# Kernel optimization log

Measured on AMD Instinct MI355X. Metric: run time of the kernel, lower is better.

The kernel has to match this reference:

```python
import jax, jax.numpy as jnp
import numpy as np

B, N, P, D, H = 16, 256, 8, 512, 8
E = P * D  # 4096, flattened patch embedding width


def _sincos_pos_embed(q_len, d_model):
    # PatchTST-style 'sincos' positional encoding (learn_pe=False buffer)
    pe = np.zeros((q_len, d_model), dtype=np.float64)
    position = np.arange(q_len, dtype=np.float64)[:, None]
    div_term = np.exp(np.arange(0, d_model, 2, dtype=np.float64) * -(np.log(10000.0) / d_model))
    pe[:, 0::2] = np.sin(position * div_term)
    pe[:, 1::2] = np.cos(position * div_term)
    pe = pe - pe.mean()
    pe = pe / (pe.std() * 10)
    return jnp.asarray(pe, dtype=jnp.float32)


def setup_inputs() -> dict:
    key = jax.random.key(0)
    ks = jax.random.split(key, 10)
    s = 0.02
    return {
        "x": jax.random.normal(ks[0], (B, N, P, D), dtype=jnp.float32),
        "pos_embed": _sincos_pos_embed(N, E),
        "W_embed": jax.random.normal(ks[1], (E, E), dtype=jnp.float32) * s,
        "b_embed": jnp.zeros((E,), dtype=jnp.float32),
        "Wq": jax.random.normal(ks[2], (E, E), dtype=jnp.float32) * s,
        "bq": jnp.zeros((E,), dtype=jnp.float32),
        "Wk": jax.random.normal(ks[3], (E, E), dtype=jnp.float32) * s,
        "bk": jnp.zeros((E,), dtype=jnp.float32),
        "Wv": jax.random.normal(ks[4], (E, E), dtype=jnp.float32) * s,
        "bv": jnp.zeros((E,), dtype=jnp.float32),
        "Wo": jax.random.normal(ks[5], (E, E), dtype=jnp.float32) * s,
        "bo": jnp.zeros((E,), dtype=jnp.float32),
    }


def reference(x, pos_embed, W_embed, b_embed, Wq, bq, Wk, bk, Wv, bv, Wo, bo):
    b, n, p, d = x.shape
    h = H
    dh = E // h  # per-head dim = patch_size * d_keys
    xe = x.reshape(b, n, p * d)                       # B N (P D)
    xe = xe @ W_embed.T + b_embed                     # embed_linear
    xe = xe + pos_embed                               # pos embed (dropout=0, eval)
    q = (xe @ Wq.T + bq).reshape(b, n, h, dh)
    k = (xe @ Wk.T + bk).reshape(b, n, h, dh)
    v = (xe @ Wv.T + bv).reshape(b, n, h, dh)
    scale = 1.0 / np.sqrt(d // h)                     # NOTE: uses d_model//H, not E//H (faithful)
    attn_scores = jnp.einsum('bnhd,bmhd->bhnm', q, k) * scale
    attn_weights = jax.nn.softmax(attn_scores, axis=-1)
    out = jnp.einsum('bhnm,bmhd->bnhd', attn_weights, v).reshape(b, n, h * dh)
    out = out @ Wo.T + bo
    out = out.reshape(b, n, p, d)
    return out, attn_weights
```

## Files before the change

### kernel.cpp

```cpp
#include <hip/hip_runtime.h>
#include <hip/hip_bf16.h>


typedef unsigned short u16;
typedef _Float16 f16;
typedef __attribute__((ext_vector_type(8))) _Float16 v8h;
typedef __attribute__((ext_vector_type(8))) short vu16x8;
typedef __attribute__((ext_vector_type(4))) float vf32x4;

#define MFMA_F16(a, b, c) __builtin_amdgcn_mfma_f32_16x16x32_f16(a, b, c, 0, 0, 0)

__device__ __forceinline__ void gld16(const void* g, void* l) {
    __builtin_amdgcn_global_load_lds((const __attribute__((address_space(1))) void*)g,
                                     (__attribute__((address_space(3))) void*)l,
                                     16, 0, 0);
}

__global__ __launch_bounds__(256) void tof16(const float* __restrict__ s,
                                             f16* __restrict__ d) {
    const size_t i = ((size_t)blockIdx.x * 256 + threadIdx.x) * 4;
    const float4 v = *(const float4*)(s + i);
    d[i + 0] = (f16)v.x; d[i + 1] = (f16)v.y;
    d[i + 2] = (f16)v.z; d[i + 3] = (f16)v.w;
}

template <int MODE>
__global__ __launch_bounds__(512, 2)
void gemm8_nt(const f16* __restrict__ A, const f16* __restrict__ Bw,
              const float* __restrict__ bias, const float* __restrict__ pos,
              f16* __restrict__ Ch, float* __restrict__ Cf) {
    __shared__ __align__(16) u16 sA[2][16384];
    __shared__ __align__(16) u16 sB[2][16384];
    const int t = threadIdx.x;
    const int lane = t & 63, w = t >> 6;
    const int wm = w >> 2, wn = w & 3;
    const int l15 = lane & 15, lg = lane >> 4;
    const int wg = ((blockIdx.x & 7) << 5) + (blockIdx.x >> 3);
    const int m0 = (wg >> 4) << 8, n0 = (wg & 15) << 8;

    int srow[4], scol[4];
#pragma unroll
    for (int i = 0; i < 4; ++i) {
        const int c = t + (i << 9);
        srow[i] = c >> 3;
        scol[i] = (((c & 7) ^ (srow[i] & 7)) << 3);
    }
    const int rA = (wm << 7) + l15;
    const int rB = (wn << 6) + l15;
    const int xA = rA & 7, xB = rB & 7;

    vf32x4 acc[8][4] = {};

#define STAGE(buf, k0) do {                                                    \
    _Pragma("unroll")                                                          \
    for (int i = 0; i < 4; ++i) {                                              \
        const int c = t + (i << 9);                                            \
        gld16(A  + (((size_t)(m0 + srow[i])) << 12) + (k0) + scol[i],          \
              &sA[buf][c * 8]);                                                \
    }                                                                          \
    _Pragma("unroll")                                                          \
    for (int i = 0; i < 4; ++i) {                                              \
        const int c = t + (i << 9);                                            \
        gld16(Bw + (((size_t)(n0 + srow[i])) << 12) + (k0) + scol[i],          \
              &sB[buf][c * 8]);                                                \
    }                                                                          \
} while (0)

    STAGE(0, 0);

    for (int kt = 0; kt < 64; ++kt) {
        const int cb = kt & 1;
        if (kt < 63) {
            STAGE(cb ^ 1, (kt + 1) << 6);
            asm volatile("s_waitcnt vmcnt(8)" ::: "memory");
        } else {
            asm volatile("s_waitcnt vmcnt(0)" ::: "memory");
        }
        __builtin_amdgcn_s_barrier();
        asm volatile("" ::: "memory");
#pragma unroll
        for (int kk = 0; kk < 2; ++kk) {
            const int ccA = (((kk << 2) + lg) ^ xA) << 3;
            const int ccB = (((kk << 2) + lg) ^ xB) << 3;
            v8h av[8], bv[4];
#pragma unroll
            for (int m = 0; m < 8; ++m)
                av[m] = *(const v8h*)(&sA[cb][(rA << 6) + (m << 10) + ccA]);
#pragma unroll
            for (int n = 0; n < 4; ++n)
                bv[n] = *(const v8h*)(&sB[cb][(rB << 6) + (n << 10) + ccB]);
            asm volatile("s_waitcnt lgkmcnt(0)" ::: "memory");
            __builtin_amdgcn_sched_barrier(0);
            __builtin_amdgcn_s_setprio(1);
#pragma unroll
            for (int m = 0; m < 8; ++m)
#pragma unroll
                for (int n = 0; n < 4; ++n)
                    acc[m][n] = MFMA_F16(av[m], bv[n], acc[m][n]);
            __builtin_amdgcn_s_setprio(0);
        }
        __builtin_amdgcn_s_barrier();
        asm volatile("" ::: "memory");
    }
#undef STAGE

#pragma unroll
    for (int n = 0; n < 4; ++n) {
        const int col = n0 + (wn << 6) + (n << 4) + l15;
        const float bvv = bias[col];
#pragma unroll
        for (int m = 0; m < 8; ++m) {
#pragma unroll
            for (int r = 0; r < 4; ++r) {
                const int row = m0 + (wm << 7) + (m << 4) + (lg << 2) + r;
                float v = acc[m][n][r] + bvv;
                if (MODE == 0) v += pos[((size_t)(row & 255) << 12) + col];
                if (MODE == 2)
                    Cf[((size_t)row << 12) + col] = v;
                else
                    Ch[((size_t)row << 12) + col] = (f16)v;
            }
        }
    }
}

__global__ __launch_bounds__(256)
void attn_scores(const f16* __restrict__ q, const f16* __restrict__ k,
                 float* __restrict__ Pf, f16* __restrict__ Pb) {
    const int blk = ((blockIdx.x & 7) << 6) + (blockIdx.x >> 3);
    const int bh = blk >> 2, it = blk & 3;
    const int b = bh >> 3, h = bh & 7;
    const size_t qoff = ((size_t)(b * 256 + it * 64) << 12) + (h << 9);
    const size_t koff = ((size_t)(b * 256) << 12) + (h << 9);
    __shared__ __align__(16) u16 Qs[64 * 64];
    __shared__ __align__(16) u16 Ks[256 * 64];
    __shared__ float red[4][64];

    const int t = threadIdx.x;
    const int lane = t & 63, w = t >> 6;
    const int l15 = lane & 15, lg = lane >> 4;

    vf32x4 acc[4][4] = {};

    for (int k0 = 0; k0 < 512; k0 += 64) {
#pragma unroll
        for (int i = 0; i < 2; ++i) {
            const int c = t + (i << 8);
            const int row = c >> 3, c8 = (c & 7) << 3;
            gld16(q + qoff + ((size_t)row << 12) + k0 + c8, Qs + c * 8);
        }
#pragma unroll
        for (int i = 0; i < 8; ++i) {
            const int c = t + (i << 8);
            const int row = c >> 3, c8 = (c & 7) << 3;
            gld16(k + koff + ((size_t)row << 12) + k0 + c8, Ks + c * 8);
        }
        __syncthreads();
#pragma unroll
        for (int kk = 0; kk < 2; ++kk) {
            v8h af[4], bf[4];
#pragma unroll
            for (int m = 0; m < 4; ++m)
                af[m] = *(const v8h*)(Qs + (m * 16 + l15) * 64 + kk * 32 + lg * 8);
#pragma unroll
            for (int n = 0; n < 4; ++n)
                bf[n] = *(const v8h*)(Ks + (w * 64 + n * 16 + l15) * 64 + kk * 32 + lg * 8);
#pragma unroll
            for (int m = 0; m < 4; ++m)
#pragma unroll
                for (int n = 0; n < 4; ++n)
                    acc[m][n] = MFMA_F16(af[m], bf[n], acc[m][n]);
        }
        __syncthreads();
    }

#pragma unroll
    for (int m = 0; m < 4; ++m)
#pragma unroll
        for (int n = 0; n < 4; ++n) acc[m][n] *= 0.125f;

    float gm[4][4];
#pragma unroll
    for (int m = 0; m < 4; ++m)
#pragma unroll
        for (int r = 0; r < 4; ++r) {
            float v = fmaxf(fmaxf(acc[m][0][r], acc[m][1][r]),
                            fmaxf(acc[m][2][r], acc[m][3][r]));
#pragma unroll
            for (int off = 1; off < 16; off <<= 1) v = fmaxf(v, __shfl_xor(v, off));
            gm[m][r] = v;
        }
    if (l15 == 0) {
#pragma unroll
        for (int m = 0; m < 4; ++m)
#pragma unroll
            for (int r = 0; r < 4; ++r) red[w][m * 16 + lg * 4 + r] = gm[m][r];
    }
    __syncthreads();
#pragma unroll
    for (int m = 0; m < 4; ++m)
#pragma unroll
        for (int r = 0; r < 4; ++r) {
            const int row = m * 16 + lg * 4 + r;
            gm[m][r] = fmaxf(fmaxf(red[0][row], red[1][row]),
                             fmaxf(red[2][row], red[3][row]));
        }
    __syncthreads();

    float gs[4][4];
#pragma unroll
    for (int m = 0; m < 4; ++m)
#pragma unroll
        for (int r = 0; r < 4; ++r) {
            float s = 0.f;
#pragma unroll
            for (int n = 0; n < 4; ++n) {
                const float e = __expf(acc[m][n][r] - gm[m][r]);
                acc[m][n][r] = e;
                s += e;
            }
#pragma unroll
            for (int off = 1; off < 16; off <<= 1) s += __shfl_xor(s, off);
            gs[m][r] = s;
        }
    if (l15 == 0) {
#pragma unroll
        for (int m = 0; m < 4; ++m)
#pragma unroll
            for (int r = 0; r < 4; ++r) red[w][m * 16 + lg * 4 + r] = gs[m][r];
    }
    __syncthreads();

    const size_t pbase = ((size_t)bh * 256 + it * 64) * 256;
#pragma unroll
    for (int m = 0; m < 4; ++m)
#pragma unroll
        for (int r = 0; r < 4; ++r) {
            const int row = m * 16 + lg * 4 + r;
            const float inv = 1.0f / (red[0][row] + red[1][row] +
                                      red[2][row] + red[3][row]);
#pragma unroll
            for (int n = 0; n < 4; ++n) {
                const int col = w * 64 + n * 16 + l15;
                const float p = acc[m][n][r] * inv;
                Pf[pbase + (size_t)row * 256 + col] = p;
                Pb[pbase + (size_t)row * 256 + col] = (f16)p;
            }
        }
}

__global__ __launch_bounds__(256)
void attn_pv(const f16* __restrict__ P, const f16* __restrict__ V,
             f16* __restrict__ O) {
    __shared__ __align__(16) u16 Ps[128 * 64];
    __shared__ __align__(16) u16 Vt[128 * 72];
    const int t = threadIdx.x;
    const int lane = t & 63, w = t >> 6;
    const int wr = (w >> 1) << 6, wc = (w & 1) << 6;
    const int l15 = lane & 15, lg = lane >> 4;
    const int blk = ((blockIdx.x & 7) << 7) + (blockIdx.x >> 3);
    const int bh = blk >> 3, mt = (blk >> 2) & 1, nt = blk & 3;
    const int b = bh >> 3, h = bh & 7;
    const f16* Pbp = P + ((size_t)bh << 16) + ((size_t)mt << 15);
    const u16* Vb = (const u16*)V + ((size_t)(b * 256) << 12) + (h << 9) + (nt << 7);

    vf32x4 acc[4][4] = {};

    for (int k0 = 0; k0 < 256; k0 += 64) {
#pragma unroll
        for (int i = 0; i < 4; ++i) {
            const int c = t + (i << 8);
            const int row = c >> 3, c8 = (c & 7) << 3;
            gld16(Pbp + (size_t)row * 256 + k0 + c8, Ps + c * 8);
        }
#pragma unroll
        for (int pp = 0; pp < 4; ++pp) {
            const int kr = pp * 16 + (t >> 4);
            const int c8 = (t & 15) << 3;
            vu16x8 vv = *(const vu16x8*)(Vb + ((size_t)(k0 + kr) << 12) + c8);
#pragma unroll
            for (int c = 0; c < 8; ++c) Vt[(c8 + c) * 72 + kr] = (u16)vv[c];
        }
        __syncthreads();
#pragma unroll
        for (int kk = 0; kk < 2; ++kk) {
            v8h af[4], bf[4];
#pragma unroll
            for (int m = 0; m < 4; ++m)
                af[m] = *(const v8h*)(Ps + (wr + m * 16 + l15) * 64 + kk * 32 + lg * 8);
#pragma unroll
            for (int n = 0; n < 4; ++n)
                bf[n] = *(const v8h*)(Vt + (wc + n * 16 + l15) * 72 + kk * 32 + lg * 8);
#pragma unroll
            for (int m = 0; m < 4; ++m)
#pragma unroll
                for (int n = 0; n < 4; ++n)
                    acc[m][n] = MFMA_F16(af[m], bf[n], acc[m][n]);
        }
        __syncthreads();
    }

#pragma unroll
    for (int m = 0; m < 4; ++m)
#pragma unroll
        for (int n = 0; n < 4; ++n) {
            const int col = (h << 9) + (nt << 7) + wc + n * 16 + l15;
#pragma unroll
            for (int r = 0; r < 4; ++r) {
                const int row = b * 256 + mt * 128 + wr + m * 16 + lg * 4 + r;
                O[((size_t)row << 12) + col] = (f16)acc[m][n][r];
            }
        }
}

extern "C" void kernel_launch(void* const* d_in, const int* in_sizes, int n_in,
                              void* d_out, int out_size, void* d_ws, size_t ws_size,
                              hipStream_t stream) {
    const float* x   = (const float*)d_in[0];
    const float* pos = (const float*)d_in[1];
    const float* wE  = (const float*)d_in[2];
    const float* bE  = (const float*)d_in[3];
    const float* wQ  = (const float*)d_in[4];
    const float* bq  = (const float*)d_in[5];
    const float* wK  = (const float*)d_in[6];
    const float* bk  = (const float*)d_in[7];
    const float* wV  = (const float*)d_in[8];
    const float* bv  = (const float*)d_in[9];
    const float* wO  = (const float*)d_in[10];
    const float* bo  = (const float*)d_in[11];

    float* out  = (float*)d_out;
    float* Pout = out + (size_t)16777216;

    char* W = (char*)d_ws;
    const size_t MB = 1024 * 1024;
    f16* xf    = (f16*)(W + 0 * MB);
    f16* wslab = (f16*)(W + 32 * MB);
    f16* xe    = (f16*)(W + 64 * MB);
    f16* qs    = (f16*)(W + 96 * MB);
    f16* ks    = (f16*)(W + 128 * MB);
    f16* vs    = (f16*)(W + 160 * MB);
    f16* Pb    = (f16*)(W + 192 * MB);
    f16* ao    = xf;

    const int CVG = 16384;

    tof16<<<CVG, 256, 0, stream>>>(x, xf);
    tof16<<<CVG, 256, 0, stream>>>(wE, wslab);
    gemm8_nt<0><<<256, 512, 0, stream>>>(xf, wslab, bE, pos, xe, nullptr);

    tof16<<<CVG, 256, 0, stream>>>(wQ, wslab);
    gemm8_nt<1><<<256, 512, 0, stream>>>(xe, wslab, bq, nullptr, qs, nullptr);

    tof16<<<CVG, 256, 0, stream>>>(wK, wslab);
    gemm8_nt<1><<<256, 512, 0, stream>>>(xe, wslab, bk, nullptr, ks, nullptr);

    tof16<<<CVG, 256, 0, stream>>>(wV, wslab);
    gemm8_nt<1><<<256, 512, 0, stream>>>(xe, wslab, bv, nullptr, vs, nullptr);

    attn_scores<<<512, 256, 0, stream>>>(qs, ks, Pout, Pb);
    attn_pv<<<1024, 256, 0, stream>>>(Pb, vs, ao);

    tof16<<<CVG, 256, 0, stream>>>(wO, wslab);
    gemm8_nt<2><<<256, 512, 0, stream>>>(ao, wslab, bo, nullptr, nullptr, out);
}
```

Measured before the change: 859.0 us.

## Fuse next weight's fp16 conversion into the tail of each GEMM kernel

Each projection GEMM now converts the next layer's fp32 weight to fp16 after its epilogue, so four separate tof16 launches go away. Separate weight buffers are assigned so the conversion target never aliases the weight the current GEMM is reading. q is staged in the output buffer as scratch. This trims launch overhead and lets conversion traffic overlap with compute-tail imbalance, at the cost of a longer per-block tail and extra memory use.

New measurement: 873.6 us. About the same (+1.7%).

```diff
diff --git a/kernel.cpp b/kernel.cpp
--- a/kernel.cpp
+++ b/kernel.cpp
@@ -24,11 +24,12 @@
     d[i + 2] = (f16)v.z; d[i + 3] = (f16)v.w;
 }
 
-template <int MODE>
+template <int MODE, bool CVT>
 __global__ __launch_bounds__(512, 2)
 void gemm8_nt(const f16* __restrict__ A, const f16* __restrict__ Bw,
               const float* __restrict__ bias, const float* __restrict__ pos,
-              f16* __restrict__ Ch, float* __restrict__ Cf) {
+              f16* __restrict__ Ch, float* __restrict__ Cf,
+              const float* __restrict__ cvsrc, f16* __restrict__ cvdst) {
     __shared__ __align__(16) u16 sA[2][16384];
     __shared__ __align__(16) u16 sB[2][16384];
     const int t = threadIdx.x;
@@ -120,6 +121,17 @@
                 else
                     Ch[((size_t)row << 12) + col] = (f16)v;
             }
+        }
+    }
+
+    if (CVT) {
+        const size_t g = (size_t)blockIdx.x * 512 + t;
+#pragma unroll 4
+        for (int j = 0; j < 32; ++j) {
+            const size_t i = ((size_t)j * 131072 + g) * 4;
+            const float4 v = *(const float4*)(cvsrc + i);
+            cvdst[i + 0] = (f16)v.x; cvdst[i + 1] = (f16)v.y;
+            cvdst[i + 2] = (f16)v.z; cvdst[i + 3] = (f16)v.w;
         }
     }
 }
@@ -334,33 +346,35 @@
 
     char* W = (char*)d_ws;
     const size_t MB = 1024 * 1024;
-    f16* xf    = (f16*)(W + 0 * MB);
-    f16* wslab = (f16*)(W + 32 * MB);
-    f16* xe    = (f16*)(W + 64 * MB);
-    f16* qs    = (f16*)(W + 96 * MB);
-    f16* ks    = (f16*)(W + 128 * MB);
-    f16* vs    = (f16*)(W + 160 * MB);
-    f16* Pb    = (f16*)(W + 192 * MB);
-    f16* ao    = xf;
+    f16* xf  = (f16*)(W + 0 * MB);
+    f16* wEs = (f16*)(W + 32 * MB);
+    f16* wVs = wEs;
+    f16* xe  = (f16*)(W + 64 * MB);
+    f16* wQs = (f16*)(W + 96 * MB);
+    f16* ao  = wQs;
+    f16* wKs = (f16*)(W + 128 * MB);
+    f16* wOs = wKs;
+    f16* ks  = (f16*)(W + 160 * MB);
+    f16* vs  = (f16*)(W + 192 * MB);
+    f16* Pb  = (f16*)(W + 224 * MB);
+    f16* qs  = (f16*)out;
 
     const int CVG = 16384;
 
     tof16<<<CVG, 256, 0, stream>>>(x, xf);
-    tof16<<<CVG, 256, 0, stream>>>(wE, wslab);
-    gemm8_nt<0><<<256, 512, 0, stream>>>(xf, wslab, bE, pos, xe, nullptr);
-
-    tof16<<<CVG, 256, 0, stream>>>(wQ, wslab);
-    gemm8_nt<1><<<256, 512, 0, stream>>>(xe, wslab, bq, nullptr, qs, nullptr);
-
-    tof16<<<CVG, 256, 0, stream>>>(wK, wslab);
-    gemm8_nt<1><<<256, 512, 0, stream>>>(xe, wslab, bk, nullptr, ks, nullptr);
-
-    tof16<<<CVG, 256, 0, stream>>>(wV, wslab);
-    gemm8_nt<1><<<256, 512, 0, stream>>>(xe, wslab, bv, nullptr, vs, nullptr);
+    tof16<<<CVG, 256, 0, stream>>>(wE, wEs);
+    gemm8_nt<0, true><<<256, 512, 0, stream>>>(xf, wEs, bE, pos, xe, nullptr,
+                                               wQ, wQs);
+    gemm8_nt<1, true><<<256, 512, 0, stream>>>(xe, wQs, bq, nullptr, qs, nullptr,
+                                               wK, wKs);
+    gemm8_nt<1, true><<<256, 512, 0, stream>>>(xe, wKs, bk, nullptr, ks, nullptr,
+                                               wV, wVs);
+    gemm8_nt<1, true><<<256, 512, 0, stream>>>(xe, wVs, bv, nullptr, vs, nullptr,
+                                               wO, wOs);
 
     attn_scores<<<512, 256, 0, stream>>>(qs, ks, Pout, Pb);
     attn_pv<<<1024, 256, 0, stream>>>(Pb, vs, ao);
 
-    tof16<<<CVG, 256, 0, stream>>>(wO, wslab);
-    gemm8_nt<2><<<256, 512, 0, stream>>>(ao, wslab, bo, nullptr, nullptr, out);
-}
+    gemm8_nt<2, false><<<256, 512, 0, stream>>>(ao, wOs, bo, nullptr, nullptr, out,
+                                                nullptr, nullptr);
+}
```

## Use smaller 256x128 tile GEMM with more blocks for QKV projections

Applied to the files above, without the earlier changes.

Adds a gemm4_nt kernel with a 256x128 output tile and 512 blocks, replacing the 256x256 tile kernel for the Q, K and V projections. The aim is more resident blocks per CU, so that one block's loads overlap with another's compute, and better wave balance. In exchange it drops the in-block double buffering and waits on all loads before each k-step, which exposes global load latency within a block. It also lowers arithmetic intensity per tile.

Result: no change. 845.6 us (-1.6%).

```diff
diff --git a/kernel.cpp b/kernel.cpp
--- a/kernel.cpp
+++ b/kernel.cpp
@@ -51,7 +51,7 @@
 
     vf32x4 acc[8][4] = {};
 
-#define STAGE(buf, k0) do {                                                    \
+#define STAGE8(buf, k0) do {                                                   \
     _Pragma("unroll")                                                          \
     for (int i = 0; i < 4; ++i) {                                              \
         const int c = t + (i << 9);                                            \
@@ -66,12 +66,12 @@
     }                                                                          \
 } while (0)
 
-    STAGE(0, 0);
+    STAGE8(0, 0);
 
     for (int kt = 0; kt < 64; ++kt) {
         const int cb = kt & 1;
         if (kt < 63) {
-            STAGE(cb ^ 1, (kt + 1) << 6);
+            STAGE8(cb ^ 1, (kt + 1) << 6);
             asm volatile("s_waitcnt vmcnt(8)" ::: "memory");
         } else {
             asm volatile("s_waitcnt vmcnt(0)" ::: "memory");
@@ -102,7 +102,7 @@
         __builtin_amdgcn_s_barrier();
         asm volatile("" ::: "memory");
     }
-#undef STAGE
+#undef STAGE8
 
 #pragma unroll
     for (int n = 0; n < 4; ++n) {
@@ -119,6 +119,94 @@
                     Cf[((size_t)row << 12) + col] = v;
                 else
                     Ch[((size_t)row << 12) + col] = (f16)v;
+            }
+        }
+    }
+}
+
+__global__ __launch_bounds__(512, 4)
+void gemm4_nt(const f16* __restrict__ A, const f16* __restrict__ Bw,
+              const float* __restrict__ bias, f16* __restrict__ Ch) {
+    __shared__ __align__(16) u16 sA[16384];
+    __shared__ __align__(16) u16 sB[8192];
+    const int t = threadIdx.x;
+    const int lane = t & 63, w = t >> 6;
+    const int wm = w >> 1, wn = w & 1;
+    const int l15 = lane & 15, lg = lane >> 4;
+    const int wg = ((blockIdx.x & 7) << 6) + (blockIdx.x >> 3);
+    const int m0 = (wg >> 5) << 8, n0 = (wg & 31) << 7;
+
+    int aRow[4], aCol[4], bRow[2], bCol[2];
+#pragma unroll
+    for (int i = 0; i < 4; ++i) {
+        const int c = t + (i << 9);
+        aRow[i] = c >> 3;
+        aCol[i] = (((c & 7) ^ (aRow[i] & 7)) << 3);
+    }
+#pragma unroll
+    for (int i = 0; i < 2; ++i) {
+        const int c = t + (i << 9);
+        bRow[i] = c >> 3;
+        bCol[i] = (((c & 7) ^ (bRow[i] & 7)) << 3);
+    }
+    const int rA = (wm << 6) + l15;
+    const int rB = (wn << 6) + l15;
+    const int xA = rA & 7, xB = rB & 7;
+
+    vf32x4 acc[4][4] = {};
+
+    for (int kt = 0; kt < 64; ++kt) {
+        const int k0 = kt << 6;
+#pragma unroll
+        for (int i = 0; i < 4; ++i) {
+            const int c = t + (i << 9);
+            gld16(A + (((size_t)(m0 + aRow[i])) << 12) + k0 + aCol[i],
+                  &sA[c * 8]);
+        }
+#pragma unroll
+        for (int i = 0; i < 2; ++i) {
+            const int c = t + (i << 9);
+            gld16(Bw + (((size_t)(n0 + bRow[i])) << 12) + k0 + bCol[i],
+                  &sB[c * 8]);
+        }
+        asm volatile("s_waitcnt vmcnt(0)" ::: "memory");
+        __builtin_amdgcn_s_barrier();
+        asm volatile("" ::: "memory");
+#pragma unroll
+        for (int kk = 0; kk < 2; ++kk) {
+            const int ccA = (((kk << 2) + lg) ^ xA) << 3;
+            const int ccB = (((kk << 2) + lg) ^ xB) << 3;
+            v8h av[4], bv[4];
+#pragma unroll
+            for (int m = 0; m < 4; ++m)
+                av[m] = *(const v8h*)(&sA[(rA << 6) + (m << 10) + ccA]);
+#pragma unroll
+            for (int n = 0; n < 4; ++n)
+                bv[n] = *(const v8h*)(&sB[(rB << 6) + (n << 10) + ccB]);
+            asm volatile("s_waitcnt lgkmcnt(0)" ::: "memory");
+            __builtin_amdgcn_sched_barrier(0);
+            __builtin_amdgcn_s_setprio(1);
+#pragma unroll
+            for (int m = 0; m < 4; ++m)
+#pragma unroll
+                for (int n = 0; n < 4; ++n)
+                    acc[m][n] = MFMA_F16(av[m], bv[n], acc[m][n]);
+            __builtin_amdgcn_s_setprio(0);
+        }
+        __builtin_amdgcn_s_barrier();
+        asm volatile("" ::: "memory");
+    }
+
+#pragma unroll
+    for (int n = 0; n < 4; ++n) {
+        const int col = n0 + (wn << 6) + (n << 4) + l15;
+        const float bvv = bias[col];
+#pragma unroll
+        for (int m = 0; m < 4; ++m) {
+#pragma unroll
+            for (int r = 0; r < 4; ++r) {
+                const int row = m0 + (wm << 6) + (m << 4) + (lg << 2) + r;
+                Ch[((size_t)row << 12) + col] = (f16)(acc[m][n][r] + bvv);
             }
         }
     }
@@ -350,13 +438,13 @@
     gemm8_nt<0><<<256, 512, 0, stream>>>(xf, wslab, bE, pos, xe, nullptr);
 
     tof16<<<CVG, 256, 0, stream>>>(wQ, wslab);
-    gemm8_nt<1><<<256, 512, 0, stream>>>(xe, wslab, bq, nullptr, qs, nullptr);
+    gemm4_nt<<<512, 512, 0, stream>>>(xe, wslab, bq, qs);
 
     tof16<<<CVG, 256, 0, stream>>>(wK, wslab);
-    gemm8_nt<1><<<256, 512, 0, stream>>>(xe, wslab, bk, nullptr, ks, nullptr);
+    gemm4_nt<<<512, 512, 0, stream>>>(xe, wslab, bk, ks);
 
     tof16<<<CVG, 256, 0, stream>>>(wV, wslab);
-    gemm8_nt<1><<<256, 512, 0, stream>>>(xe, wslab, bv, nullptr, vs, nullptr);
+    gemm4_nt<<<512, 512, 0, stream>>>(xe, wslab, bv, vs);
 
     attn_scores<<<512, 256, 0, stream>>>(qs, ks, Pout, Pb);
     attn_pv<<<1024, 256, 0, stream>>>(Pb, vs, ao);
```

## Shrink GEMM tiles to 256x128 with k-step 32 for higher occupancy

Applied to the files above, without the earlier changes.

Rewrites the fp16 MFMA GEMM to use 256x128 output tiles with a 32-wide k step, halving LDS use and launching 512 blocks instead of 256. Launch bounds allow 4 blocks per CU and each warp holds a 4x4 accumulator grid. It also changes the swizzled LDS staging layout to fit the smaller k slice. The aim is to fill all CUs and hide latency through occupancy, at the cost of less data reuse per tile and more barriers per unit of work.

New measurement: 914.9 us. +6.5%, slower.

```diff
diff --git a/kernel.cpp b/kernel.cpp
--- a/kernel.cpp
+++ b/kernel.cpp
@@ -25,94 +25,96 @@
 }
 
 template <int MODE>
-__global__ __launch_bounds__(512, 2)
-void gemm8_nt(const f16* __restrict__ A, const f16* __restrict__ Bw,
+__global__ __launch_bounds__(512, 4)
+void gemmd_nt(const f16* __restrict__ A, const f16* __restrict__ Bw,
               const float* __restrict__ bias, const float* __restrict__ pos,
               f16* __restrict__ Ch, float* __restrict__ Cf) {
-    __shared__ __align__(16) u16 sA[2][16384];
-    __shared__ __align__(16) u16 sB[2][16384];
+    __shared__ __align__(16) u16 sA[2][8192];
+    __shared__ __align__(16) u16 sB[2][4096];
     const int t = threadIdx.x;
     const int lane = t & 63, w = t >> 6;
-    const int wm = w >> 2, wn = w & 3;
+    const int wm = w >> 1, wn = w & 1;
     const int l15 = lane & 15, lg = lane >> 4;
-    const int wg = ((blockIdx.x & 7) << 5) + (blockIdx.x >> 3);
-    const int m0 = (wg >> 4) << 8, n0 = (wg & 15) << 8;
-
-    int srow[4], scol[4];
-#pragma unroll
-    for (int i = 0; i < 4; ++i) {
+    const int wg = ((blockIdx.x & 7) << 6) + (blockIdx.x >> 3);
+    const int m0 = (wg >> 5) << 8, n0 = (wg & 31) << 7;
+
+    int aRow[2], aCol[2];
+#pragma unroll
+    for (int i = 0; i < 2; ++i) {
         const int c = t + (i << 9);
-        srow[i] = c >> 3;
-        scol[i] = (((c & 7) ^ (srow[i] & 7)) << 3);
-    }
-    const int rA = (wm << 7) + l15;
+        const int lr = c >> 3;
+        const int v = (c & 7) ^ (lr & 7);
+        aRow[i] = ((v >> 2) << 7) + lr;
+        aCol[i] = (v & 3) << 3;
+    }
+    int bRow, bCol;
+    {
+        const int c = t;
+        const int lr = c >> 3;
+        const int v = (c & 7) ^ (lr & 7);
+        bRow = ((v >> 2) << 6) + lr;
+        bCol = (v & 3) << 3;
+    }
+    const int rA = (wm << 6) + l15;
     const int rB = (wn << 6) + l15;
-    const int xA = rA & 7, xB = rB & 7;
-
-    vf32x4 acc[8][4] = {};
-
-#define STAGE(buf, k0) do {                                                    \
+    const int cA = ((((wm >> 1) << 2) + lg) ^ (rA & 7)) << 3;
+    const int cB = (((wn << 2) + lg) ^ (rB & 7)) << 3;
+    const int lrA = ((wm & 1) << 6) + l15;
+    const int lrB = l15;
+
+    vf32x4 acc[4][4] = {};
+
+#define STG(buf, k0) do {                                                      \
     _Pragma("unroll")                                                          \
-    for (int i = 0; i < 4; ++i) {                                              \
-        const int c = t + (i << 9);                                            \
-        gld16(A  + (((size_t)(m0 + srow[i])) << 12) + (k0) + scol[i],          \
-              &sA[buf][c * 8]);                                                \
-    }                                                                          \
-    _Pragma("unroll")                                                          \
-    for (int i = 0; i < 4; ++i) {                                              \
-        const int c = t + (i << 9);                                            \
-        gld16(Bw + (((size_t)(n0 + srow[i])) << 12) + (k0) + scol[i],          \
-              &sB[buf][c * 8]);                                                \
-    }                                                                          \
+    for (int i = 0; i < 2; ++i)                                                \
+        gld16(A + (((size_t)(m0 + aRow[i])) << 12) + (k0) + aCol[i],           \
+              &sA[buf][(t + (i << 9)) * 8]);                                   \
+    gld16(Bw + (((size_t)(n0 + bRow)) << 12) + (k0) + bCol,                    \
+          &sB[buf][t * 8]);                                                    \
 } while (0)
 
-    STAGE(0, 0);
-
-    for (int kt = 0; kt < 64; ++kt) {
+    STG(0, 0);
+
+    for (int kt = 0; kt < 128; ++kt) {
         const int cb = kt & 1;
-        if (kt < 63) {
-            STAGE(cb ^ 1, (kt + 1) << 6);
-            asm volatile("s_waitcnt vmcnt(8)" ::: "memory");
+        if (kt < 127) {
+            STG(cb ^ 1, (kt + 1) << 5);
+            asm volatile("s_waitcnt vmcnt(3)" ::: "memory");
         } else {
             asm volatile("s_waitcnt vmcnt(0)" ::: "memory");
         }
         __builtin_amdgcn_s_barrier();
         asm volatile("" ::: "memory");
-#pragma unroll
-        for (int kk = 0; kk < 2; ++kk) {
-            const int ccA = (((kk << 2) + lg) ^ xA) << 3;
-            const int ccB = (((kk << 2) + lg) ^ xB) << 3;
-            v8h av[8], bv[4];
-#pragma unroll
-            for (int m = 0; m < 8; ++m)
-                av[m] = *(const v8h*)(&sA[cb][(rA << 6) + (m << 10) + ccA]);
+        v8h av[4], bv[4];
+#pragma unroll
+        for (int m = 0; m < 4; ++m)
+            av[m] = *(const v8h*)(&sA[cb][((lrA + m * 16) << 6) + cA]);
+#pragma unroll
+        for (int n = 0; n < 4; ++n)
+            bv[n] = *(const v8h*)(&sB[cb][((lrB + n * 16) << 6) + cB]);
+        asm volatile("s_waitcnt lgkmcnt(0)" ::: "memory");
+        __builtin_amdgcn_sched_barrier(0);
+        __builtin_amdgcn_s_setprio(1);
+#pragma unroll
+        for (int m = 0; m < 4; ++m)
 #pragma unroll
             for (int n = 0; n < 4; ++n)
-                bv[n] = *(const v8h*)(&sB[cb][(rB << 6) + (n << 10) + ccB]);
-            asm volatile("s_waitcnt lgkmcnt(0)" ::: "memory");
-            __builtin_amdgcn_sched_barrier(0);
-            __builtin_amdgcn_s_setprio(1);
-#pragma unroll
-            for (int m = 0; m < 8; ++m)
-#pragma unroll
-                for (int n = 0; n < 4; ++n)
-                    acc[m][n] = MFMA_F16(av[m], bv[n], acc[m][n]);
-            __builtin_amdgcn_s_setprio(0);
-        }
+                acc[m][n] = MFMA_F16(av[m], bv[n], acc[m][n]);
+        __builtin_amdgcn_s_setprio(0);
         __builtin_amdgcn_s_barrier();
         asm volatile("" ::: "memory");
     }
-#undef STAGE
+#undef STG
 
 #pragma unroll
     for (int n = 0; n < 4; ++n) {
         const int col = n0 + (wn << 6) + (n << 4) + l15;
         const float bvv = bias[col];
 #pragma unroll
-        for (int m = 0; m < 8; ++m) {
+        for (int m = 0; m < 4; ++m) {
 #pragma unroll
             for (int r = 0; r < 4; ++r) {
-                const int row = m0 + (wm << 7) + (m << 4) + (lg << 2) + r;
+                const int row = m0 + (wm << 6) + (m << 4) + (lg << 2) + r;
                 float v = acc[m][n][r] + bvv;
                 if (MODE == 0) v += pos[((size_t)(row & 255) << 12) + col];
                 if (MODE == 2)
@@ -347,20 +349,20 @@
 
     tof16<<<CVG, 256, 0, stream>>>(x, xf);
     tof16<<<CVG, 256, 0, stream>>>(wE, wslab);
-    gemm8_nt<0><<<256, 512, 0, stream>>>(xf, wslab, bE, pos, xe, nullptr);
+    gemmd_nt<0><<<512, 512, 0, stream>>>(xf, wslab, bE, pos, xe, nullptr);
 
     tof16<<<CVG, 256, 0, stream>>>(wQ, wslab);
-    gemm8_nt<1><<<256, 512, 0, stream>>>(xe, wslab, bq, nullptr, qs, nullptr);
+    gemmd_nt<1><<<512, 512, 0, stream>>>(xe, wslab, bq, nullptr, qs, nullptr);
 
     tof16<<<CVG, 256, 0, stream>>>(wK, wslab);
-    gemm8_nt<1><<<256, 512, 0, stream>>>(xe, wslab, bk, nullptr, ks, nullptr);
+    gemmd_nt<1><<<512, 512, 0, stream>>>(xe, wslab, bk, nullptr, ks, nullptr);
 
     tof16<<<CVG, 256, 0, stream>>>(wV, wslab);
-    gemm8_nt<1><<<256, 512, 0, stream>>>(xe, wslab, bv, nullptr, vs, nullptr);
+    gemmd_nt<1><<<512, 512, 0, stream>>>(xe, wslab, bv, nullptr, vs, nullptr);
 
     attn_scores<<<512, 256, 0, stream>>>(qs, ks, Pout, Pb);
     attn_pv<<<1024, 256, 0, stream>>>(Pb, vs, ao);
 
     tof16<<<CVG, 256, 0, stream>>>(wO, wslab);
-    gemm8_nt<2><<<256, 512, 0, stream>>>(ao, wslab, bo, nullptr, nullptr, out);
-}
+    gemmd_nt<2><<<512, 512, 0, stream>>>(ao, wslab, bo, nullptr, nullptr, out);
+}
```
